# Performance work log

Measured on AMD Instinct MI355X. Metric: run time of the kernel, lower is better.

Reference implementation:

```python
import jax, jax.numpy as jnp
import numpy as np
import math

B, N, M = 128, 32, 64           # batch, num_agents, num_other
OBS, ACT = 128, 16              # obs_input_dim, num_actions
D_QK = 128                      # obs_output_dim (== obs_output_dim_other)
D_AV = 64                       # obs_act_output_dim (== other)
F_IN = OBS + ACT                # obs_act_input_dim = 144


def _xavier(key, shape):
    fan_in, fan_out = shape[0], shape[1]
    limit = math.sqrt(6.0 / (fan_in + fan_out))
    return jax.random.uniform(key, shape, jnp.float32, -limit, limit)


def setup_inputs() -> dict:
    key = jax.random.key(0)
    ks = jax.random.split(key, 13)
    return {
        "states": jax.random.normal(ks[0], (B, N, OBS), jnp.float32),
        "policies": jax.random.uniform(ks[1], (B, N, ACT), jnp.float32),
        "actions": jax.random.uniform(ks[2], (B, N, ACT), jnp.float32),
        "states_other": jax.random.normal(ks[3], (B, M, OBS), jnp.float32),
        "actions_other": jax.random.uniform(ks[4], (B, M, ACT), jnp.float32),
        # weights stored as [in, out] (x @ W == nn.Linear without bias)
        "W_key": _xavier(ks[5], (OBS, D_QK)),
        "W_query": _xavier(ks[6], (OBS, D_QK)),
        "W_av": _xavier(ks[7], (F_IN, D_AV)),
        "W_key_other": _xavier(ks[8], (OBS, D_QK)),
        "W_query_other": _xavier(ks[9], (OBS, D_QK)),
        "W_av_other": _xavier(ks[10], (F_IN, D_AV)),
        "W_f1": _xavier(ks[11], (2 * D_AV, 64)),
        "W_f2": _xavier(ks[12], (64, 1)),
    }


def reference(states, policies, actions, states_other, actions_other,
              W_key, W_query, W_av, W_key_other, W_query_other,
              W_av_other, W_f1, W_f2):
    b, n, _ = states.shape
    obs_actions = jnp.concatenate([states, actions], axis=-1)   # [B,N,F_IN]
    obs_policy = jnp.concatenate([states, policies], axis=-1)   # [B,N,F_IN]

    key_obs = states @ W_key                                    # [B,N,D_QK]
    query_obs = states @ W_query                                # [B,N,D_QK]
    d_k = W_key.shape[1]
    weight = jax.nn.softmax(
        jnp.einsum('bid,bjd->bij', query_obs, key_obs) / math.sqrt(d_k), axis=-1)
    ret_weight = weight

    # place_policies is identity on (j,k): oap[b,j,k] = obs_policy[b,k] if j==k else obs_actions[b,k]
    eye = jnp.eye(n, dtype=states.dtype)[None, :, :, None]       # [1,N,N,1]
    oap = eye * obs_policy[:, None, :, :] + (1.0 - eye) * obs_actions[:, None, :, :]
    attention_values = jnp.tanh(oap @ W_av)                      # [B,N,N,D_AV] (j,k)

    # repeat-mul-sum == weighted reduction over k: wav[b,i,j,d] = sum_k w[b,i,k] av[b,j,k,d]
    wav = jnp.einsum('bik,bjkd->bijd', weight, attention_values)  # [B,N,N,D_AV]

    obs_actions_other = jnp.concatenate([states_other, actions_other], axis=-1)
    keys_other = states_other @ W_key_other                      # [B,M,D_QK]
    query_agent = states @ W_query_other                         # [B,N,D_QK]
    av_other = jnp.tanh(obs_actions_other @ W_av_other)          # [B,M,D_AV]
    d_k_o = W_key_other.shape[1]
    weight_other = jax.nn.softmax(
        jnp.einsum('bid,bmd->bim', query_agent, keys_other) / math.sqrt(d_k_o), axis=-1)
    wav_other = jnp.einsum('bim,bmd->bid', weight_other, av_other)  # [B,N,D_AV]

    # broadcast the per-agent other-branch features across the j axis for the concat
    wav_other_b = jnp.broadcast_to(wav_other[:, :, None, :], wav.shape[:-1] + (wav_other.shape[-1],))
    node_features = jnp.concatenate([wav, wav_other_b], axis=-1)  # [B,N,N,2*D_AV]

    h = jax.nn.leaky_relu(node_features @ W_f1, negative_slope=0.01)
    value = h @ W_f2                                              # [B,N,N,1]
    return value, ret_weight, weight_other
```

## Files before the change

### kernel.cpp

```cpp
#include <hip/hip_runtime.h>
#include <math.h>

#define WS_WQK   0
#define WS_WQKO  16384
#define WS_AVA   32768
#define WS_AVO   294912
#define WS_DPROJ 819200

#define INV_SQRT_DK 0.08838834764831845f

#define SWZ32(row, c) (((c) ^ ((row) >> 3)) & 31)
#define SWZ16(row, c) (((c) ^ ((row) >> 3)) & 15)

__device__ __forceinline__ float dot4(float4 a, float4 b) {
  return a.x*b.x + a.y*b.y + a.z*b.z + a.w*b.w;
}
__device__ __forceinline__ void fma4(float4& a, const float4 w, const float s) {
  a.x += w.x*s; a.y += w.y*s; a.z += w.z*s; a.w += w.w*s;
}

__global__ __launch_bounds__(256, 2) void k1_pre(
    const float* __restrict__ g_states, const float* __restrict__ g_pol,
    const float* __restrict__ g_act, const float* __restrict__ g_so,
    const float* __restrict__ g_ao,
    const float* __restrict__ Wq, const float* __restrict__ Wk,
    const float* __restrict__ Wqo, const float* __restrict__ Wko,
    const float* __restrict__ W_av, const float* __restrict__ W_avo,
    const float* __restrict__ W_f1, float* __restrict__ ws)
{
  __shared__ __align__(16) float pool[8448];
  const int t = threadIdx.x;
  int blk = blockIdx.x;

  if (blk < 32) {
    const float* A; const float* Bm; float* O;
    if (blk < 16) { A = Wq;  Bm = Wk;  O = ws + WS_WQK; }
    else          { A = Wqo; Bm = Wko; O = ws + WS_WQKO; blk -= 16; }
    const int tr = (blk >> 2) << 5;
    const int tc = (blk & 3) << 5;
    float* sA = pool;
    float* sB = pool + 4224;
    const float4* a4 = (const float4*)(A + tr * 128);
    const float4* b4 = (const float4*)(Bm + tc * 128);
    #pragma unroll
    for (int u = 0; u < 4; ++u) {
      int f = t + u * 256;
      int r = f >> 5, c4 = f & 31;
      *(float4*)(sA + r*132 + c4*4) = a4[f];
      *(float4*)(sB + r*132 + c4*4) = b4[f];
    }
    __syncthreads();
    const int e = t & 31, cl0 = t >> 5;
    float acc[4] = {0,0,0,0};
    #pragma unroll 4
    for (int d4 = 0; d4 < 32; ++d4) {
      float4 bv = *(const float4*)(sB + e*132 + d4*4);
      #pragma unroll
      for (int rr = 0; rr < 4; ++rr) {
        float4 av = *(const float4*)(sA + (cl0 + rr*8)*132 + d4*4);
        acc[rr] += dot4(av, bv);
      }
    }
    #pragma unroll
    for (int rr = 0; rr < 4; ++rr)
      O[(tr + cl0 + rr*8)*128 + tc + e] = acc[rr];
    return;
  }
  blk -= 32;

  if (blk < 512) {
    const int b  = blk >> 2;
    const int jq = blk & 3;
    float* s_in  = pool;
    float* s_t   = pool + 1056;
    float* s_pre = pool + 1376;
    float* s_dl  = pool + 2432;
    {
      const float4* gs4 = (const float4*)(g_states + b*4096 + jq*1024);
      int r = t >> 5, c4 = t & 31;
      *(float4*)(s_in + r*132 + c4*4) = gs4[t];
      if (t < 32) {
        int rr = t >> 2, cc = t & 3;
        *(float4*)(s_t + rr*40 + cc*4) =
            ((const float4*)(g_act + b*512 + jq*128))[t];
      } else if (t < 64) {
        int t2 = t - 32;
        int rr = t2 >> 2, cc = t2 & 3;
        *(float4*)(s_t + rr*40 + 20 + cc*4) =
            ((const float4*)(g_pol + b*512 + jq*128))[t2];
      }
    }
    __syncthreads();
    {
      const int wv_  = t >> 6;
      const int ap   = wv_ & 1;
      const int rq   = wv_ >> 1;
      const int lane = t & 63;
      const float* s_rows = s_in + rq*4*132;
      const float* s_tl   = s_t + rq*4*40 + ap*20;
      float acc[4] = {0,0,0,0};
      #pragma unroll 4
      for (int c4 = 0; c4 < 32; ++c4) {
        const float w0 = W_av[(c4*4+0)*64 + lane];
        const float w1 = W_av[(c4*4+1)*64 + lane];
        const float w2 = W_av[(c4*4+2)*64 + lane];
        const float w3 = W_av[(c4*4+3)*64 + lane];
        #pragma unroll
        for (int r = 0; r < 4; ++r) {
          float4 sv = *(const float4*)(s_rows + r*132 + c4*4);
          acc[r] += sv.x*w0 + sv.y*w1 + sv.z*w2 + sv.w*w3;
        }
      }
      #pragma unroll
      for (int c4 = 0; c4 < 4; ++c4) {
        const float w0 = W_av[(128 + c4*4+0)*64 + lane];
        const float w1 = W_av[(128 + c4*4+1)*64 + lane];
        const float w2 = W_av[(128 + c4*4+2)*64 + lane];
        const float w3 = W_av[(128 + c4*4+3)*64 + lane];
        #pragma unroll
        for (int r = 0; r < 4; ++r) {
          float4 sv = *(const float4*)(s_tl + r*40 + c4*4);
          acc[r] += sv.x*w0 + sv.y*w1 + sv.z*w2 + sv.w*w3;
        }
      }
      #pragma unroll
      for (int r = 0; r < 4; ++r)
        s_pre[(rq*4 + r)*132 + ap*64 + lane] = acc[r];
    }
    __syncthreads();
    if (t < 128) {
      const int r = t >> 4, d0 = (t & 15) << 2;
      float4 a0 = *(const float4*)(s_pre + r*132 + d0);
      float4 p0 = *(const float4*)(s_pre + r*132 + 64 + d0);
      float4 va0, dl0;
      va0.x = tanhf(a0.x); va0.y = tanhf(a0.y); va0.z = tanhf(a0.z); va0.w = tanhf(a0.w);
      dl0.x = tanhf(p0.x) - va0.x; dl0.y = tanhf(p0.y) - va0.y;
      dl0.z = tanhf(p0.z) - va0.z; dl0.w = tanhf(p0.w) - va0.w;
      *(float4*)(ws + WS_AVA + b*2048 + (jq*8 + r)*64 + d0) = va0;
      *(float4*)(s_dl + r*68 + d0) = dl0;
    }
    __syncthreads();
    {
      const int h = t & 63;
      const int j0 = (t >> 6) << 1;
      float acc[2] = {0,0};
      #pragma unroll 4
      for (int d4 = 0; d4 < 16; ++d4) {
        float w0 = W_f1[(d4*4+0)*64 + h];
        float w1 = W_f1[(d4*4+1)*64 + h];
        float w2 = W_f1[(d4*4+2)*64 + h];
        float w3 = W_f1[(d4*4+3)*64 + h];
        #pragma unroll
        for (int q = 0; q < 2; ++q) {
          float4 dv = *(const float4*)(s_dl + (j0+q)*68 + d4*4);
          acc[q] += dv.x*w0 + dv.y*w1 + dv.z*w2 + dv.w*w3;
        }
      }
      #pragma unroll
      for (int q = 0; q < 2; ++q)
        ws[WS_DPROJ + b*2048 + (jq*8 + j0+q)*64 + h] = acc[q];
    }
    return;
  }
  blk -= 512;

  {
    const int b = blk >> 2, m0 = (blk & 3) << 4;
    float* s_so = pool;
    float* s_ao = pool + 2112;
    {
      const float4* gso4 = (const float4*)(g_so + (b*64 + m0) * 128);
      #pragma unroll
      for (int u = 0; u < 2; ++u) {
        int f = t + u * 256;
        int r = f >> 5, c4 = f & 31;
        *(float4*)(s_so + r*132 + c4*4) = gso4[f];
      }
      if (t < 64) {
        int r = t >> 2, c4 = t & 3;
        *(float4*)(s_ao + r*20 + c4*4) =
            ((const float4*)(g_ao + (b*64 + m0)*16))[t];
      }
    }
    __syncthreads();
    const int wv_  = t >> 6;
    const int lane = t & 63;
    const float* s_rows = s_so + wv_*4*132;
    const float* s_tl   = s_ao + wv_*4*20;
    float acc[4] = {0.f, 0.f, 0.f, 0.f};
    #pragma unroll 4
    for (int c4 = 0; c4 < 32; ++c4) {
      const float w0 = W_avo[(c4*4+0)*64 + lane];
      const float w1 = W_avo[(c4*4+1)*64 + lane];
      const float w2 = W_avo[(c4*4+2)*64 + lane];
      const float w3 = W_avo[(c4*4+3)*64 + lane];
      #pragma unroll
      for (int r = 0; r < 4; ++r) {
        float4 sv = *(const float4*)(s_rows + r*132 + c4*4);
        acc[r] += sv.x*w0 + sv.y*w1 + sv.z*w2 + sv.w*w3;
      }
    }
    #pragma unroll
    for (int c4 = 0; c4 < 4; ++c4) {
      const float w0 = W_avo[(128 + c4*4+0)*64 + lane];
      const float w1 = W_avo[(128 + c4*4+1)*64 + lane];
      const float w2 = W_avo[(128 + c4*4+2)*64 + lane];
      const float w3 = W_avo[(128 + c4*4+3)*64 + lane];
      #pragma unroll
      for (int r = 0; r < 4; ++r) {
        float4 sv = *(const float4*)(s_tl + r*20 + c4*4);
        acc[r] += sv.x*w0 + sv.y*w1 + sv.z*w2 + sv.w*w3;
      }
    }
    #pragma unroll
    for (int r = 0; r < 4; ++r)
      ws[WS_AVO + b*4096 + (m0 + wv_*4 + r)*64 + lane] = tanhf(acc[r]);
  }
}

__global__ __launch_bounds__(512, 2) void k2_main(
    const float* __restrict__ g_states, const float* __restrict__ g_so,
    const float* __restrict__ W_f1, const float* __restrict__ W_f2,
    const float* __restrict__ ws, float* __restrict__ out)
{
  __shared__ __align__(16) float pool[17472];
  float* s_st   = pool;
  float* s_red  = pool + 4352;
  float* s_so   = pool + 4352;
  float* s_avA  = pool + 4352;
  float* s_dp   = pool + 6528;
  float* s_avO  = pool;
  float* s_P    = pool + 12800;
  float* s_w    = pool + 14944;
  float* s_wo   = pool + 15232;
  float* s_S    = pool + 15776;
  float* s_wavo = pool + 16320;
  float* s_base = pool + 16864;
  float* s_wf2  = pool + 17408;

  const int t = threadIdx.x;
  const int b = blockIdx.x >> 2;
  const int i0 = (blockIdx.x & 3) << 3;

  {
    const float4* gs4 = (const float4*)(g_states + b * 4096);
    #pragma unroll
    for (int u = 0; u < 2; ++u) {
      int f = t + u * 512;
      int r = f >> 5, c4 = f & 31;
      *(float4*)(s_st + r*132 + 4*SWZ32(r, c4)) = gs4[f];
    }
    if (t < 16) *(float4*)(s_wf2 + t*4) = ((const float4*)W_f2)[t];
  }
  __syncthreads();

  {
    const int wave = t >> 6;
    const int kc   = wave & 3;
    const int rh   = wave >> 2;
    const int col  = t & 63;
    const float* Wp = (col < 32) ? (ws + WS_WQK + col*4)
                                 : (ws + WS_WQKO + (col-32)*4);
    const int rbase = i0 + rh*4;
    const int rsw   = i0 >> 3;
    float4 acc[4];
    #pragma unroll
    for (int r = 0; r < 4; ++r) acc[r] = make_float4(0.f,0.f,0.f,0.f);
    #pragma unroll 2
    for (int c4 = 0; c4 < 8; ++c4) {
      const int colw = 4*(((kc*8 + c4) ^ rsw) & 31);
      float4 sv[4];
      #pragma unroll
      for (int r = 0; r < 4; ++r)
        sv[r] = *(const float4*)(s_st + (rbase + r)*132 + colw);
      #pragma unroll
      for (int k = 0; k < 4; ++k) {
        float4 wv = *(const float4*)(Wp + (kc*32 + c4*4 + k)*128);
        #pragma unroll
        for (int r = 0; r < 4; ++r)
          fma4(acc[r], wv, ((const float*)&sv[r])[k]);
      }
    }
    #pragma unroll
    for (int r = 0; r < 4; ++r)
      *(float4*)(s_red + ((kc*8 + rh*4 + r)*66 + col)*4) = acc[r];
  }
  __syncthreads();
  {
    const int r = t >> 6, col = t & 63;
    float4 a0 = *(const float4*)(s_red + ((0*8 + r)*66 + col)*4);
    float4 a1 = *(const float4*)(s_red + ((1*8 + r)*66 + col)*4);
    float4 a2 = *(const float4*)(s_red + ((2*8 + r)*66 + col)*4);
    float4 a3 = *(const float4*)(s_red + ((3*8 + r)*66 + col)*4);
    float4 s4;
    s4.x = (a0.x + a1.x) + (a2.x + a3.x);
    s4.y = (a0.y + a1.y) + (a2.y + a3.y);
    s4.z = (a0.z + a1.z) + (a2.z + a3.z);
    s4.w = (a0.w + a1.w) + (a2.w + a3.w);
    *(float4*)(s_P + r*268 + col*4) = s4;
  }
  __syncthreads();

  float4 stg[4];
  {
    const float4* gso4 = (const float4*)(g_so + b * 64 * 128);
    #pragma unroll
    for (int u = 0; u < 4; ++u) stg[u] = gso4[t + u*512];
  }
  {
    const int r = t >> 6, j = t & 31, half = (t >> 5) & 1;
    const int e0 = half << 4;
    float acc = 0.f;
    #pragma unroll 8
    for (int e4 = 0; e4 < 16; ++e4) {
      float4 p4  = *(const float4*)(s_P + r*268 + (e0 + e4)*4);
      float4 st4 = *(const float4*)(s_st + j*132 + 4*SWZ32(j, e0 + e4));
      acc += dot4(p4, st4);
    }
    acc += __shfl_xor(acc, 32, 64);
    acc *= INV_SQRT_DK;
    float mx = acc;
    for (int off = 16; off; off >>= 1) mx = fmaxf(mx, __shfl_xor(mx, off, 32));
    float ev = __expf(acc - mx);
    float sum = ev;
    for (int off = 16; off; off >>= 1) sum += __shfl_xor(sum, off, 32);
    float wn = ev / sum;
    if (half == 0) {
      out[131072 + b*1024 + (i0 + r)*32 + j] = wn;
      s_w[r*36 + j] = wn;
    }
  }
  {
    #pragma unroll
    for (int u = 0; u < 4; ++u) {
      int f = t + u * 512;
      int m = f >> 5, c4 = f & 31;
      *(float4*)(s_so + m*132 + 4*SWZ32(m, c4)) = stg[u];
    }
  }
  __syncthreads();

  {
    const int r = t >> 6, m = t & 63;
    float acc = 0.f;
    #pragma unroll 8
    for (int c4 = 0; c4 < 32; ++c4) {
      float4 p4  = *(const float4*)(s_P + r*268 + 128 + c4*4);
      float4 so4 = *(const float4*)(s_so + m*132 + 4*SWZ32(m, c4));
      acc += dot4(p4, so4);
    }
    s_wo[r*68 + m] = acc * INV_SQRT_DK;
  }
  __syncthreads();

  {
    const int r = t >> 6, l = t & 63;
    float v = s_wo[r*68 + l];
    float mx = v;
    for (int off = 32; off; off >>= 1) mx = fmaxf(mx, __shfl_xor(mx, off, 64));
    float ev = __expf(v - mx);
    float sum = ev;
    for (int off = 32; off; off >>= 1) sum += __shfl_xor(sum, off, 64);
    float wn = ev / sum;
    out[262144 + b*2048 + (i0 + r)*64 + l] = wn;
    s_wo[r*68 + l] = wn;
  }
  {
    int k = t >> 4, dq = t & 15;
    *(float4*)(s_avA + k*68 + dq*4) = ((const float4*)(ws + WS_AVA + b*2048))[t];
    *(float4*)(s_dp  + k*68 + 4*SWZ16(k, dq)) =
        ((const float4*)(ws + WS_DPROJ + b*2048))[t];
  }
  #pragma unroll
  for (int u = 0; u < 2; ++u) {
    int f = t + u * 512;
    int m = f >> 4, dq = f & 15;
    *(float4*)(s_avO + m*68 + dq*4) = ((const float4*)(ws + WS_AVO + b*4096))[f];
  }
  __syncthreads();

  if (t < 128) {
    const int i = t >> 4, dq = (t & 15) << 2;
    float4 acc = {0,0,0,0};
    #pragma unroll 4
    for (int k = 0; k < 32; ++k) {
      float4 a4 = *(const float4*)(s_avA + k*68 + dq);
      float wv = s_w[i*36 + k];
      acc.x += wv*a4.x; acc.y += wv*a4.y; acc.z += wv*a4.z; acc.w += wv*a4.w;
    }
    *(float4*)(s_S + i*68 + dq) = acc;
  } else if (t < 384) {
    const int tt2 = t - 128;
    const int mh = tt2 >> 7;
    const int i = (tt2 & 127) >> 4, dq = (tt2 & 15) << 2;
    float4 acc = {0,0,0,0};
    #pragma unroll 4
    for (int mm = 0; mm < 32; ++mm) {
      const int m = mh*32 + mm;
      float4 a4 = *(const float4*)(s_avO + m*68 + dq);
      float wv = s_wo[i*68 + m];
      acc.x += wv*a4.x; acc.y += wv*a4.y; acc.z += wv*a4.z; acc.w += wv*a4.w;
    }
    float* dst = mh ? (s_P + i*68 + dq) : (s_wavo + i*68 + dq);
    *(float4*)dst = acc;
  }
  __syncthreads();

  {
    const int h = t & 63, i = t >> 6;
    float a0 = 0.f;
    #pragma unroll 4
    for (int d = 0; d < 64; ++d) {
      float w1v = W_f1[d*64 + h];
      float w2v = W_f1[(64 + d)*64 + h];
      a0 += s_S[i*68 + d]*w1v + (s_wavo[i*68 + d] + s_P[i*68 + d])*w2v;
    }
    s_base[i*68 + h] = a0;
  }
  __syncthreads();

  {
    const int i = t >> 6, j = t & 31, half = (t >> 5) & 1;
    const float wij = s_w[i*36 + j];
    float acc = 0.f;
    #pragma unroll 4
    for (int hq = half*8; hq < half*8 + 8; ++hq) {
      float4 b4 = *(const float4*)(s_base + i*68 + hq*4);
      float4 d4 = *(const float4*)(s_dp + j*68 + 4*SWZ16(j, hq));
      float4 f4 = *(const float4*)(s_wf2 + hq*4);
      float p0 = b4.x + wij*d4.x; p0 = p0 > 0.f ? p0 : 0.01f*p0;
      float p1 = b4.y + wij*d4.y; p1 = p1 > 0.f ? p1 : 0.01f*p1;
      float p2 = b4.z + wij*d4.z; p2 = p2 > 0.f ? p2 : 0.01f*p2;
      float p3 = b4.w + wij*d4.w; p3 = p3 > 0.f ? p3 : 0.01f*p3;
      acc += p0*f4.x + p1*f4.y + p2*f4.z + p3*f4.w;
    }
    acc += __shfl_xor(acc, 32, 64);
    if (half == 0)
      out[b*1024 + (i0 + i)*32 + j] = acc;
  }
}

extern "C" void kernel_launch(void* const* d_in, const int* in_sizes, int n_in,
                              void* d_out, int out_size, void* d_ws, size_t ws_size,
                              hipStream_t stream) {
  const float* states        = (const float*)d_in[0];
  const float* policies      = (const float*)d_in[1];
  const float* actions       = (const float*)d_in[2];
  const float* states_other  = (const float*)d_in[3];
  const float* actions_other = (const float*)d_in[4];
  const float* W_key         = (const float*)d_in[5];
  const float* W_query       = (const float*)d_in[6];
  const float* W_av          = (const float*)d_in[7];
  const float* W_key_other   = (const float*)d_in[8];
  const float* W_query_other = (const float*)d_in[9];
  const float* W_av_other    = (const float*)d_in[10];
  const float* W_f1          = (const float*)d_in[11];
  const float* W_f2          = (const float*)d_in[12];
  float* out = (float*)d_out;
  float* ws  = (float*)d_ws;

  k1_pre<<<1056, 256, 0, stream>>>(states, policies, actions, states_other,
                                   actions_other, W_query, W_key,
                                   W_query_other, W_key_other, W_av, W_av_other,
                                   W_f1, ws);
  k2_main<<<512, 512, 0, stream>>>(states, states_other, W_f1, W_f2, ws, out);
}
```

Baseline: 114.5 us.

## Reduce projection K-splits with wave shuffles and prefetch workspace tiles early

The split-K reduction of the Q/K projection in k2_main now runs inside each wave. Lanes are regrouped so the four K-chunks share a wave and are combined with __shfl_xor, which removes a shared-memory scratch round-trip and one __syncthreads. The states_other load and the workspace tiles (avA, dproj, avO) are issued into registers earlier so their global latency overlaps compute. The cost is more live registers per thread under launch_bounds(512,2), which could raise register pressure.

```diff
diff --git a/kernel.cpp b/kernel.cpp
--- a/kernel.cpp
+++ b/kernel.cpp
@@ -225,7 +225,6 @@
 {
   __shared__ __align__(16) float pool[17472];
   float* s_st   = pool;
-  float* s_red  = pool + 4352;
   float* s_so   = pool + 4352;
   float* s_avA  = pool + 4352;
   float* s_dp   = pool + 6528;
@@ -242,6 +241,13 @@
   const int b = blockIdx.x >> 2;
   const int i0 = (blockIdx.x & 3) << 3;
 
+  float4 stg[4];
+  {
+    const float4* gso4 = (const float4*)(g_so + b * 64 * 128);
+    #pragma unroll
+    for (int u = 0; u < 4; ++u) stg[u] = gso4[t + u*512];
+  }
+
   {
     const float4* gs4 = (const float4*)(g_states + b * 4096);
     #pragma unroll
@@ -255,10 +261,13 @@
   __syncthreads();
 
   {
-    const int wave = t >> 6;
-    const int kc   = wave & 3;
-    const int rh   = wave >> 2;
-    const int col  = t & 63;
+    const int wave   = t >> 6;
+    const int colgrp = wave & 3;
+    const int rh     = wave >> 2;
+    const int lane   = t & 63;
+    const int kc     = lane >> 4;
+    const int colsub = lane & 15;
+    const int col    = colgrp*16 + colsub;
     const float* Wp = (col < 32) ? (ws + WS_WQK + col*4)
                                  : (ws + WS_WQKO + (col-32)*4);
     const int rbase = i0 + rh*4;
@@ -282,31 +291,32 @@
       }
     }
     #pragma unroll
-    for (int r = 0; r < 4; ++r)
-      *(float4*)(s_red + ((kc*8 + rh*4 + r)*66 + col)*4) = acc[r];
-  }
-  __syncthreads();
-  {
-    const int r = t >> 6, col = t & 63;
-    float4 a0 = *(const float4*)(s_red + ((0*8 + r)*66 + col)*4);
-    float4 a1 = *(const float4*)(s_red + ((1*8 + r)*66 + col)*4);
-    float4 a2 = *(const float4*)(s_red + ((2*8 + r)*66 + col)*4);
-    float4 a3 = *(const float4*)(s_red + ((3*8 + r)*66 + col)*4);
-    float4 s4;
-    s4.x = (a0.x + a1.x) + (a2.x + a3.x);
-    s4.y = (a0.y + a1.y) + (a2.y + a3.y);
-    s4.z = (a0.z + a1.z) + (a2.z + a3.z);
-    s4.w = (a0.w + a1.w) + (a2.w + a3.w);
-    *(float4*)(s_P + r*268 + col*4) = s4;
-  }
-  __syncthreads();
-
-  float4 stg[4];
-  {
-    const float4* gso4 = (const float4*)(g_so + b * 64 * 128);
-    #pragma unroll
-    for (int u = 0; u < 4; ++u) stg[u] = gso4[t + u*512];
-  }
+    for (int r = 0; r < 4; ++r) {
+      acc[r].x += __shfl_xor(acc[r].x, 16, 64);
+      acc[r].y += __shfl_xor(acc[r].y, 16, 64);
+      acc[r].z += __shfl_xor(acc[r].z, 16, 64);
+      acc[r].w += __shfl_xor(acc[r].w, 16, 64);
+      acc[r].x += __shfl_xor(acc[r].x, 32, 64);
+      acc[r].y += __shfl_xor(acc[r].y, 32, 64);
+      acc[r].z += __shfl_xor(acc[r].z, 32, 64);
+      acc[r].w += __shfl_xor(acc[r].w, 32, 64);
+    }
+    if (kc == 0) {
+      #pragma unroll
+      for (int r = 0; r < 4; ++r)
+        *(float4*)(s_P + (rh*4 + r)*268 + col*4) = acc[r];
+    }
+  }
+
+  float4 pA, pD, pO0, pO1;
+  {
+    pA  = ((const float4*)(ws + WS_AVA   + b*2048))[t];
+    pD  = ((const float4*)(ws + WS_DPROJ + b*2048))[t];
+    pO0 = ((const float4*)(ws + WS_AVO   + b*4096))[t];
+    pO1 = ((const float4*)(ws + WS_AVO   + b*4096))[t + 512];
+  }
+  __syncthreads();
+
   {
     const int r = t >> 6, j = t & 31, half = (t >> 5) & 1;
     const int e0 = half << 4;
@@ -367,15 +377,12 @@
   }
   {
     int k = t >> 4, dq = t & 15;
-    *(float4*)(s_avA + k*68 + dq*4) = ((const float4*)(ws + WS_AVA + b*2048))[t];
-    *(float4*)(s_dp  + k*68 + 4*SWZ16(k, dq)) =
-        ((const float4*)(ws + WS_DPROJ + b*2048))[t];
-  }
-  #pragma unroll
-  for (int u = 0; u < 2; ++u) {
-    int f = t + u * 512;
-    int m = f >> 4, dq = f & 15;
-    *(float4*)(s_avO + m*68 + dq*4) = ((const float4*)(ws + WS_AVO + b*4096))[f];
+    *(float4*)(s_avA + k*68 + dq*4) = pA;
+    *(float4*)(s_dp  + k*68 + 4*SWZ16(k, dq)) = pD;
+    int m0 = t >> 4;
+    *(float4*)(s_avO + m0*68 + dq*4) = pO0;
+    int m1 = (t + 512) >> 4;
+    *(float4*)(s_avO + m1*68 + dq*4) = pO1;
   }
   __syncthreads();
 
```

After: 117.9 us. 3.0% more time.
